# Kernel optimization log

Hardware: AMD Instinct MI355X
Metric: run time of the kernel (lower is better)

The kernel has to match this reference:

```python
import jax, jax.numpy as jnp
import numpy as np

N_EMBD = 768
N_HEAD = 12
HEAD_DIM = N_EMBD // N_HEAD


def setup_inputs() -> dict:
    key = jax.random.key(0)
    ks = jax.random.split(key, 9)
    s = 0.02
    return {
        "x": jax.random.normal(ks[0], (2, 4096, N_EMBD), dtype=jnp.float32),
        "Wq": jax.random.normal(ks[1], (N_EMBD, N_EMBD), dtype=jnp.float32) * s,
        "bq": jnp.zeros((N_EMBD,), dtype=jnp.float32),
        "Wk": jax.random.normal(ks[2], (N_EMBD, N_EMBD), dtype=jnp.float32) * s,
        "bk": jnp.zeros((N_EMBD,), dtype=jnp.float32),
        "Wv": jax.random.normal(ks[3], (N_EMBD, N_EMBD), dtype=jnp.float32) * s,
        "bv": jnp.zeros((N_EMBD,), dtype=jnp.float32),
        "Wo": jax.random.normal(ks[4], (N_EMBD, N_EMBD), dtype=jnp.float32) * s,
        "bo": jnp.zeros((N_EMBD,), dtype=jnp.float32),
    }


def reference(x, Wq, bq, Wk, bk, Wv, bv, Wo, bo):
    B, T, C = x.shape
    H, D = N_HEAD, HEAD_DIM
    # torch Linear: y = x @ W.T + b
    q = (x @ Wq.T + bq).reshape(B, T, H, D).transpose(0, 2, 1, 3)  # [B,H,T,D]
    k = (x @ Wk.T + bk).reshape(B, T, H, D).transpose(0, 2, 1, 3)
    v = (x @ Wv.T + bv).reshape(B, T, H, D).transpose(0, 2, 1, 3)
    scale = 1.0 / jnp.sqrt(jnp.float32(D))
    att = jnp.einsum("bhqd,bhkd->bhqk", q, k) * scale  # [B,H,T,T]
    causal = jnp.tril(jnp.ones((T, T), dtype=bool))
    att = jnp.where(causal[None, None], att, -jnp.inf)
    att = jax.nn.softmax(att, axis=-1)
    y = jnp.einsum("bhqk,bhkd->bhqd", att, v)
    y = y.transpose(0, 2, 1, 3).reshape(B, T, C)
    return y @ Wo.T + bo
```

## Files before the change

kernel.cpp:

```cpp
#include <hip/hip_runtime.h>

typedef __bf16 bf16_t;
typedef __bf16 bf16x4 __attribute__((ext_vector_type(4)));
typedef __bf16 bf16x8 __attribute__((ext_vector_type(8)));
typedef float  f32x4  __attribute__((ext_vector_type(4)));
typedef float  f32x16 __attribute__((ext_vector_type(16)));
typedef unsigned int u32;

#define MFMA16(a, b, c) __builtin_amdgcn_mfma_f32_16x16x32_bf16((a), (b), (c), 0, 0, 0)
#define MFMA32(a, b, c) __builtin_amdgcn_mfma_f32_32x32x16_bf16((a), (b), (c), 0, 0, 0)

__device__ __forceinline__ void gld_lds16(const bf16_t* g, bf16_t* l) {
  __builtin_amdgcn_global_load_lds((__attribute__((address_space(1))) void*)g,
                                   (__attribute__((address_space(3))) void*)l, 16, 0, 0);
}
__device__ __forceinline__ u32 cvt_pk_bf16(float lo, float hi) {
  u32 r;
  asm("v_cvt_pk_bf16_f32 %0, %1, %2" : "=v"(r) : "v"(lo), "v"(hi));
  return r;
}

__global__ void cast_f32_bf16(const float* __restrict__ s, bf16_t* __restrict__ d, int n) {
  int i = (blockIdx.x * blockDim.x + threadIdx.x) * 4;
  if (i >= n) return;
  float4 v = *(const float4*)(s + i);
  bf16x4 o;
  o[0] = (bf16_t)v.x; o[1] = (bf16_t)v.y; o[2] = (bf16_t)v.z; o[3] = (bf16_t)v.w;
  *(bf16x4*)(d + i) = o;
}

__global__ void prep_w(const float* __restrict__ Wq, const float* __restrict__ Wk,
                       const float* __restrict__ Wv, const float* __restrict__ Wo,
                       const float* __restrict__ bq, const float* __restrict__ bk,
                       const float* __restrict__ bv,
                       bf16_t* __restrict__ wqkv, bf16_t* __restrict__ wob,
                       float* __restrict__ qkvb) {
  const int NW = 768 * 768;
  const int t = blockIdx.x * 256 + threadIdx.x;
  const int i = t * 4;
  if (i < 3 * NW) {
    const float* s; int off;
    if (i < NW)          { s = Wq; off = i; }
    else if (i < 2 * NW) { s = Wk; off = i - NW; }
    else                 { s = Wv; off = i - 2 * NW; }
    float4 v = *(const float4*)(s + off);
    bf16x4 o;
    o[0] = (bf16_t)v.x; o[1] = (bf16_t)v.y; o[2] = (bf16_t)v.z; o[3] = (bf16_t)v.w;
    *(bf16x4*)(wqkv + i) = o;
  } else if (i < 4 * NW) {
    const int off = i - 3 * NW;
    float4 v = *(const float4*)(Wo + off);
    bf16x4 o;
    o[0] = (bf16_t)v.x; o[1] = (bf16_t)v.y; o[2] = (bf16_t)v.z; o[3] = (bf16_t)v.w;
    *(bf16x4*)(wob + off) = o;
  }
  if (t < 2304) qkvb[t] = t < 768 ? bq[t] : (t < 1536 ? bk[t - 768] : bv[t - 1536]);
}

__global__ __launch_bounds__(256) void gemm_qkv(
    const bf16_t* __restrict__ A, const bf16_t* __restrict__ B,
    const float* __restrict__ bias,
    bf16_t* __restrict__ qb, bf16_t* __restrict__ kb2, bf16_t* __restrict__ vtb) {
  __shared__ __align__(16) bf16_t As[128 * 64];
  __shared__ __align__(16) bf16_t Bs[128 * 64];
  const int K = 768;
  const int bm = blockIdx.x, bn = blockIdx.y;
  const int tid = threadIdx.x;
  const int w = tid >> 6, l = tid & 63, lg = l >> 4, ln = l & 15;
  const int wr = w >> 1, wc = w & 1;
  const int lr8 = l >> 3, lc8 = l & 7;
  const int region = (bn * 128) / 768;
  const int ln7 = ln & 7;
  f32x4 acc[4][4] = {};
  for (int kb = 0; kb < K / 64; ++kb) {
    const int k0 = kb * 64;
#pragma unroll
    for (int i = 0; i < 4; ++i) {
      const int row = w * 32 + i * 8 + lr8;
      const int so = k0 + ((lc8 ^ (row & 7)) << 3);
      gld_lds16(A + (size_t)(bm * 128 + row) * K + so, As + (w * 32 + i * 8) * 64 + l * 8);
      gld_lds16(B + (size_t)(bn * 128 + row) * K + so, Bs + (w * 32 + i * 8) * 64 + l * 8);
    }
    __syncthreads();
#pragma unroll
    for (int kk = 0; kk < 2; ++kk) {
      bf16x8 af[4], bfr[4];
#pragma unroll
      for (int m = 0; m < 4; ++m) {
        const int jc = ((kk * 4 + lg) ^ ln7) << 3;
        af[m]  = *(const bf16x8*)(As + (wr * 64 + m * 16 + ln) * 64 + jc);
        bfr[m] = *(const bf16x8*)(Bs + (wc * 64 + m * 16 + ln) * 64 + jc);
      }
      if (region != 2) {
#pragma unroll
        for (int m = 0; m < 4; ++m)
#pragma unroll
          for (int n = 0; n < 4; ++n) acc[m][n] = MFMA16(af[m], bfr[n], acc[m][n]);
      } else {
#pragma unroll
        for (int m = 0; m < 4; ++m)
#pragma unroll
          for (int n = 0; n < 4; ++n) acc[m][n] = MFMA16(bfr[n], af[m], acc[m][n]);
      }
    }
    __syncthreads();
  }
  if (region != 2) {
    const float scl = (region == 0) ? 0.18033688011112042f : 1.0f;
    bf16_t* dst = region == 0 ? qb : kb2;
#pragma unroll
    for (int m = 0; m < 4; ++m)
#pragma unroll
      for (int n = 0; n < 4; ++n)
#pragma unroll
        for (int j = 0; j < 4; ++j) {
          const int gm = bm * 128 + wr * 64 + m * 16 + lg * 4 + j;
          const int gn = bn * 128 + wc * 64 + n * 16 + ln;
          const float v = (acc[m][n][j] + bias[gn]) * scl;
          const int c = gn - region * 768;
          const int bb = gm >> 12, tt = gm & 4095;
          const int hh = c >> 6, d = c & 63;
          dst[((size_t)(bb * 12 + hh) * 4096 + tt) * 64 + d] = (bf16_t)v;
        }
  } else {
#pragma unroll
    for (int m = 0; m < 4; ++m)
#pragma unroll
      for (int n = 0; n < 4; ++n)
#pragma unroll
        for (int j = 0; j < 4; ++j) {
          const int gn = bn * 128 + wc * 64 + n * 16 + lg * 4 + j;
          const int gm = bm * 128 + wr * 64 + m * 16 + ln;
          const float v = acc[m][n][j] + bias[gn];
          const int c = gn - 1536;
          const int bb = gm >> 12, tt = gm & 4095;
          const int hh = c >> 6, d = c & 63;
          vtb[((size_t)(bb * 12 + hh) * 64 + d) * 4096 + tt] = (bf16_t)v;
        }
  }
}

__global__ __launch_bounds__(512) void attn_fwd(
    const bf16_t* __restrict__ q, const bf16_t* __restrict__ k,
    const bf16_t* __restrict__ vt, bf16_t* __restrict__ y) {
  __shared__ __align__(16) unsigned char SMEM[65536];
  bf16_t* Ks = (bf16_t*)SMEM;
  bf16_t* Vs = (bf16_t*)(SMEM + 32768);
  float*  osh = (float*)SMEM;
  float*  lsh = (float*)(SMEM + 32768);

  const int p = blockIdx.x;
  const int xcd = p & 7, slot = p >> 3;
  const int hb = xcd + 8 * (slot % 3);
  const int qt = 31 - slot / 3;
  const int tid = threadIdx.x;
  const int w = tid >> 6, l = tid & 63, lq = l & 31, lh = l >> 5;
  const int wq = w >> 1, wc = w & 1;
  const size_t hbo = (size_t)hb * (4096 * 64);
  const bf16_t* qh = q + hbo;
  const bf16_t* kh = k + hbo;
  const bf16_t* vh = vt + hbo;

  const int q0 = qt * 128 + wq * 32;
  const int qidx = q0 + lq;
  const int nst = qt + 1;

  const int sr = ((tid >> 8) << 5) | (tid & 31);
  const int sc = ((((tid >> 6) & 3) << 1) | ((tid >> 5) & 1)) << 3;
  const bf16_t* k0src = kh + ((size_t)sr * 64 + sc);
  const bf16_t* k1src = k0src + 4096;
  const bf16_t* v0src = vh + ((size_t)sr * 4096 + sc);
  const bf16_t* v1src = v0src + 64;

  bf16x8 qf[4];
#pragma unroll
  for (int ds = 0; ds < 4; ++ds)
    qf[ds] = *(const bf16x8*)(qh + (size_t)qidx * 64 + 16 * ds + 8 * lh);

  gld_lds16(k0src, Ks + tid * 8);
  gld_lds16(k1src, Ks + 4096 + tid * 8);
  gld_lds16(v0src, Vs + tid * 8);
  gld_lds16(v1src, Vs + 4096 + tid * 8);
  __syncthreads();

  f32x16 o0 = {}, o1 = {};
  float lsum = 0.f;

  int cur = 0;
  for (int i = 0; i < nst; ++i) {
    if (i + 1 < nst) {
      bf16_t* kd = Ks + (cur ^ 1) * 8192;
      bf16_t* vd = Vs + (cur ^ 1) * 8192;
      gld_lds16(k0src + 8192, kd + tid * 8);
      gld_lds16(k1src + 8192, kd + 4096 + tid * 8);
      gld_lds16(v0src + 128, vd + tid * 8);
      gld_lds16(v1src + 128, vd + 4096 + tid * 8);
    }
    k0src += 8192; k1src += 8192; v0src += 128; v1src += 128;
    const int t = 2 * i + wc;
    if (t * 64 <= q0 + 31) {
      const int kvb = t * 64;
      const bool diag = (kvb + 63 > q0);
      const bf16_t* KsW = Ks + (cur * 2 + wc) * 4096;
      const bf16_t* VsW = Vs + (cur * 2 + wc) * 4096;
      u32 pq[2][8];
#pragma unroll
      for (int kb = 0; kb < 2; ++kb) {
        f32x16 st = {};
        __builtin_amdgcn_s_setprio(1);
#pragma unroll
        for (int ds = 0; ds < 4; ++ds) {
          bf16x8 kf = *(const bf16x8*)(KsW + (kb * 4 + ds) * 512 + l * 8);
          st = MFMA32(kf, qf[ds], st);
        }
        __builtin_amdgcn_s_setprio(0);
        float pv[16];
#pragma unroll
        for (int r = 0; r < 16; ++r) pv[r] = __builtin_amdgcn_exp2f(st[r]);
        if (diag) {
          const int kb0 = kvb + kb * 32 + 4 * lh;
#pragma unroll
          for (int r = 0; r < 16; ++r)
            if (kb0 + (r & 3) + 8 * (r >> 2) > qidx) pv[r] = 0.f;
        }
#pragma unroll
        for (int r = 0; r < 16; ++r) lsum += pv[r];
#pragma unroll
        for (int g = 0; g < 8; ++g) pq[kb][g] = cvt_pk_bf16(pv[2 * g], pv[2 * g + 1]);
#pragma unroll
        for (int ks2 = 0; ks2 < 2; ++ks2) {
          asm("v_permlane32_swap_b32 %0, %1" : "+v"(pq[kb][4 * ks2 + 0]), "+v"(pq[kb][4 * ks2 + 2]));
          asm("v_permlane32_swap_b32 %0, %1" : "+v"(pq[kb][4 * ks2 + 1]), "+v"(pq[kb][4 * ks2 + 3]));
        }
      }
      __builtin_amdgcn_s_setprio(1);
#pragma unroll
      for (int ks = 0; ks < 4; ++ks) {
        bf16x8 pa = *(const bf16x8*)&pq[ks >> 1][(ks & 1) * 4];
        bf16x8 v0 = *(const bf16x8*)(VsW + ks * 512 + l * 8);
        bf16x8 v1 = *(const bf16x8*)(VsW + (4 + ks) * 512 + l * 8);
        o0 = MFMA32(pa, v0, o0);
        o1 = MFMA32(pa, v1, o1);
      }
      __builtin_amdgcn_s_setprio(0);
    }
    __syncthreads();
    cur ^= 1;
  }
  lsum += __shfl_xor(lsum, 32);

  if (wc == 1) {
#pragma unroll
    for (int r = 0; r < 16; ++r) {
      osh[wq * 2048 + r * 64 + l] = o0[r];
      osh[wq * 2048 + (16 + r) * 64 + l] = o1[r];
    }
    lsh[wq * 64 + l] = lsum;
  }
  __syncthreads();
  if (wc == 0) {
    lsum += lsh[wq * 64 + l];
#pragma unroll
    for (int r = 0; r < 16; ++r) {
      o0[r] += osh[wq * 2048 + r * 64 + l];
      o1[r] += osh[wq * 2048 + (16 + r) * 64 + l];
    }
    float linv[16];
#pragma unroll
    for (int r = 0; r < 16; ++r)
      linv[r] = 1.0f / __shfl(lsum, (r & 3) + 8 * (r >> 2) + 4 * lh);
    const int b = hb / 12, h = hb - b * 12;
#pragma unroll
    for (int r = 0; r < 16; ++r) {
      const int row = q0 + (r & 3) + 8 * (r >> 2) + 4 * lh;
      bf16_t* yr = y + ((size_t)b * 4096 + row) * 768 + h * 64 + lq;
      yr[0]  = (bf16_t)(o0[r] * linv[r]);
      yr[32] = (bf16_t)(o1[r] * linv[r]);
    }
  }
}

__global__ __launch_bounds__(256) void gemm_out(
    const bf16_t* __restrict__ A, const bf16_t* __restrict__ B,
    const float* __restrict__ bias, float* __restrict__ out) {
  __shared__ __align__(16) bf16_t As[128 * 64];
  __shared__ __align__(16) bf16_t Bs[128 * 64];
  const int K = 768;
  const int bm = blockIdx.x, bn = blockIdx.y;
  const int tid = threadIdx.x;
  const int w = tid >> 6, l = tid & 63, lg = l >> 4, ln = l & 15;
  const int wr = w >> 1, wc = w & 1;
  const int lr8 = l >> 3, lc8 = l & 7;
  const int ln7 = ln & 7;
  f32x4 acc[4][4] = {};
  for (int kb = 0; kb < K / 64; ++kb) {
    const int k0 = kb * 64;
#pragma unroll
    for (int i = 0; i < 4; ++i) {
      const int row = w * 32 + i * 8 + lr8;
      const int so = k0 + ((lc8 ^ (row & 7)) << 3);
      gld_lds16(A + (size_t)(bm * 128 + row) * K + so, As + (w * 32 + i * 8) * 64 + l * 8);
      gld_lds16(B + (size_t)(bn * 128 + row) * K + so, Bs + (w * 32 + i * 8) * 64 + l * 8);
    }
    __syncthreads();
#pragma unroll
    for (int kk = 0; kk < 2; ++kk) {
      bf16x8 af[4], bfr[4];
#pragma unroll
      for (int m = 0; m < 4; ++m) {
        const int jc = ((kk * 4 + lg) ^ ln7) << 3;
        af[m]  = *(const bf16x8*)(As + (wr * 64 + m * 16 + ln) * 64 + jc);
        bfr[m] = *(const bf16x8*)(Bs + (wc * 64 + m * 16 + ln) * 64 + jc);
      }
#pragma unroll
      for (int m = 0; m < 4; ++m)
#pragma unroll
        for (int n = 0; n < 4; ++n) acc[m][n] = MFMA16(af[m], bfr[n], acc[m][n]);
    }
    __syncthreads();
  }
  const int gn0 = bn * 128 + wc * 64;
#pragma unroll
  for (int m = 0; m < 4; ++m) {
#pragma unroll
    for (int n = 0; n < 4; ++n) {
#pragma unroll
      for (int j = 0; j < 4; ++j) {
        const int gm = bm * 128 + wr * 64 + m * 16 + lg * 4 + j;
        const int gn = gn0 + n * 16 + ln;
        out[(size_t)gm * 768 + gn] = acc[m][n][j] + bias[gn];
      }
    }
  }
}

extern "C" void kernel_launch(void* const* d_in, const int* in_sizes, int n_in,
                              void* d_out, int out_size, void* d_ws, size_t ws_size,
                              hipStream_t stream) {
  const float* x  = (const float*)d_in[0];
  const float* Wq = (const float*)d_in[1];
  const float* bq = (const float*)d_in[2];
  const float* Wk = (const float*)d_in[3];
  const float* bk = (const float*)d_in[4];
  const float* Wv = (const float*)d_in[5];
  const float* bv = (const float*)d_in[6];
  const float* Wo = (const float*)d_in[7];
  const float* bo = (const float*)d_in[8];
  float* out = (float*)d_out;

  const int M = 8192, C = 768, QKV = 2304;
  bf16_t* xb   = (bf16_t*)d_ws;
  bf16_t* wqkv = xb + (size_t)M * C;
  bf16_t* wob  = wqkv + (size_t)QKV * C;
  float*  qkvb = (float*)(wob + (size_t)C * C);
  bf16_t* qbuf = (bf16_t*)(qkvb + QKV);
  bf16_t* kbuf = qbuf + (size_t)M * C;
  bf16_t* vtb  = kbuf + (size_t)M * C;
  bf16_t* yb   = xb;

  cast_f32_bf16<<<6144, 256, 0, stream>>>(x, xb, M * C);
  prep_w<<<2304, 256, 0, stream>>>(Wq, Wk, Wv, Wo, bq, bk, bv, wqkv, wob, qkvb);

  gemm_qkv<<<dim3(64, 18), 256, 0, stream>>>(xb, wqkv, qkvb, qbuf, kbuf, vtb);
  attn_fwd<<<768, 512, 0, stream>>>(qbuf, kbuf, vtb, yb);
  gemm_out<<<dim3(64, 6), 256, 0, stream>>>(yb, wob, bo, out);
}
```

Before: 173.2 us.

## Drop split-KV wave pairs in attention; use 4 waves per block over all KV tiles

The attention kernel previously used 8 waves where pairs of waves split each 128-key stage between two 64-key halves, then reduced their partial outputs through shared memory. It now uses 4 waves per block, each covering a 32-row query slice, and walks every 64-key tile serially with a smaller double-buffered K/V staging area. This removes the cross-wave LDS reduction and final barrier and halves shared memory per block, which may allow more resident blocks. In exchange each wave does twice as many sequential iterations, with more barriers per block and less intra-block parallelism.

```diff
diff --git a/kernel.cpp b/kernel.cpp
--- a/kernel.cpp
+++ b/kernel.cpp
@@ -140,14 +140,11 @@
   }
 }
 
-__global__ __launch_bounds__(512) void attn_fwd(
+__global__ __launch_bounds__(256) void attn_fwd(
     const bf16_t* __restrict__ q, const bf16_t* __restrict__ k,
     const bf16_t* __restrict__ vt, bf16_t* __restrict__ y) {
-  __shared__ __align__(16) unsigned char SMEM[65536];
-  bf16_t* Ks = (bf16_t*)SMEM;
-  bf16_t* Vs = (bf16_t*)(SMEM + 32768);
-  float*  osh = (float*)SMEM;
-  float*  lsh = (float*)(SMEM + 32768);
+  __shared__ __align__(16) bf16_t Ks[2][4096];
+  __shared__ __align__(16) bf16_t Vs[2][4096];
 
   const int p = blockIdx.x;
   const int xcd = p & 7, slot = p >> 3;
@@ -155,54 +152,50 @@
   const int qt = 31 - slot / 3;
   const int tid = threadIdx.x;
   const int w = tid >> 6, l = tid & 63, lq = l & 31, lh = l >> 5;
-  const int wq = w >> 1, wc = w & 1;
   const size_t hbo = (size_t)hb * (4096 * 64);
   const bf16_t* qh = q + hbo;
   const bf16_t* kh = k + hbo;
   const bf16_t* vh = vt + hbo;
 
-  const int q0 = qt * 128 + wq * 32;
+  const int q0 = qt * 128 + w * 32;
   const int qidx = q0 + lq;
-  const int nst = qt + 1;
-
-  const int sr = ((tid >> 8) << 5) | (tid & 31);
-  const int sc = ((((tid >> 6) & 3) << 1) | ((tid >> 5) & 1)) << 3;
-  const bf16_t* k0src = kh + ((size_t)sr * 64 + sc);
-  const bf16_t* k1src = k0src + 4096;
-  const bf16_t* v0src = vh + ((size_t)sr * 4096 + sc);
-  const bf16_t* v1src = v0src + 64;
+  const int nst = 2 * qt + 2;
+
+  const int sr0 = tid & 31,           sc0 = ((((tid >> 6) & 3) << 1) | ((tid >> 5) & 1)) << 3;
+  const int sr1 = 32 | (tid & 31),    sc1 = sc0;
+  const bf16_t* ks0 = kh + ((size_t)sr0 * 64 + sc0);
+  const bf16_t* ks1 = kh + ((size_t)sr1 * 64 + sc1);
+  const bf16_t* vs0 = vh + ((size_t)sr0 * 4096 + sc0);
+  const bf16_t* vs1 = vh + ((size_t)sr1 * 4096 + sc1);
 
   bf16x8 qf[4];
 #pragma unroll
   for (int ds = 0; ds < 4; ++ds)
     qf[ds] = *(const bf16x8*)(qh + (size_t)qidx * 64 + 16 * ds + 8 * lh);
 
-  gld_lds16(k0src, Ks + tid * 8);
-  gld_lds16(k1src, Ks + 4096 + tid * 8);
-  gld_lds16(v0src, Vs + tid * 8);
-  gld_lds16(v1src, Vs + 4096 + tid * 8);
+  gld_lds16(ks0, &Ks[0][tid * 8]);
+  gld_lds16(ks1, &Ks[0][2048 + tid * 8]);
+  gld_lds16(vs0, &Vs[0][tid * 8]);
+  gld_lds16(vs1, &Vs[0][2048 + tid * 8]);
   __syncthreads();
 
   f32x16 o0 = {}, o1 = {};
   float lsum = 0.f;
 
   int cur = 0;
-  for (int i = 0; i < nst; ++i) {
-    if (i + 1 < nst) {
-      bf16_t* kd = Ks + (cur ^ 1) * 8192;
-      bf16_t* vd = Vs + (cur ^ 1) * 8192;
-      gld_lds16(k0src + 8192, kd + tid * 8);
-      gld_lds16(k1src + 8192, kd + 4096 + tid * 8);
-      gld_lds16(v0src + 128, vd + tid * 8);
-      gld_lds16(v1src + 128, vd + 4096 + tid * 8);
-    }
-    k0src += 8192; k1src += 8192; v0src += 128; v1src += 128;
-    const int t = 2 * i + wc;
-    if (t * 64 <= q0 + 31) {
-      const int kvb = t * 64;
+  for (int t = 0; t < nst; ++t) {
+    if (t + 1 < nst) {
+      gld_lds16(ks0 + 4096, &Ks[cur ^ 1][tid * 8]);
+      gld_lds16(ks1 + 4096, &Ks[cur ^ 1][2048 + tid * 8]);
+      gld_lds16(vs0 + 64, &Vs[cur ^ 1][tid * 8]);
+      gld_lds16(vs1 + 64, &Vs[cur ^ 1][2048 + tid * 8]);
+    }
+    ks0 += 4096; ks1 += 4096; vs0 += 64; vs1 += 64;
+    const int kvb = t * 64;
+    if (kvb <= q0 + 31) {
       const bool diag = (kvb + 63 > q0);
-      const bf16_t* KsW = Ks + (cur * 2 + wc) * 4096;
-      const bf16_t* VsW = Vs + (cur * 2 + wc) * 4096;
+      const bf16_t* KsW = &Ks[cur][0];
+      const bf16_t* VsW = &Vs[cur][0];
       u32 pq[2][8];
 #pragma unroll
       for (int kb = 0; kb < 2; ++kb) {
@@ -248,35 +241,17 @@
     cur ^= 1;
   }
   lsum += __shfl_xor(lsum, 32);
-
-  if (wc == 1) {
-#pragma unroll
-    for (int r = 0; r < 16; ++r) {
-      osh[wq * 2048 + r * 64 + l] = o0[r];
-      osh[wq * 2048 + (16 + r) * 64 + l] = o1[r];
-    }
-    lsh[wq * 64 + l] = lsum;
-  }
-  __syncthreads();
-  if (wc == 0) {
-    lsum += lsh[wq * 64 + l];
-#pragma unroll
-    for (int r = 0; r < 16; ++r) {
-      o0[r] += osh[wq * 2048 + r * 64 + l];
-      o1[r] += osh[wq * 2048 + (16 + r) * 64 + l];
-    }
-    float linv[16];
-#pragma unroll
-    for (int r = 0; r < 16; ++r)
-      linv[r] = 1.0f / __shfl(lsum, (r & 3) + 8 * (r >> 2) + 4 * lh);
-    const int b = hb / 12, h = hb - b * 12;
-#pragma unroll
-    for (int r = 0; r < 16; ++r) {
-      const int row = q0 + (r & 3) + 8 * (r >> 2) + 4 * lh;
-      bf16_t* yr = y + ((size_t)b * 4096 + row) * 768 + h * 64 + lq;
-      yr[0]  = (bf16_t)(o0[r] * linv[r]);
-      yr[32] = (bf16_t)(o1[r] * linv[r]);
-    }
+  float linv[16];
+#pragma unroll
+  for (int r = 0; r < 16; ++r)
+    linv[r] = 1.0f / __shfl(lsum, (r & 3) + 8 * (r >> 2) + 4 * lh);
+  const int b = hb / 12, h = hb - b * 12;
+#pragma unroll
+  for (int r = 0; r < 16; ++r) {
+    const int row = q0 + (r & 3) + 8 * (r >> 2) + 4 * lh;
+    bf16_t* yr = y + ((size_t)b * 4096 + row) * 768 + h * 64 + lq;
+    yr[0]  = (bf16_t)(o0[r] * linv[r]);
+    yr[32] = (bf16_t)(o1[r] * linv[r]);
   }
 }
 
@@ -362,6 +337,6 @@
   prep_w<<<2304, 256, 0, stream>>>(Wq, Wk, Wv, Wo, bq, bk, bv, wqkv, wob, qkvb);
 
   gemm_qkv<<<dim3(64, 18), 256, 0, stream>>>(xb, wqkv, qkvb, qbuf, kbuf, vtb);
-  attn_fwd<<<768, 512, 0, stream>>>(qbuf, kbuf, vtb, yb);
+  attn_fwd<<<768, 256, 0, stream>>>(qbuf, kbuf, vtb, yb);
   gemm_out<<<dim3(64, 6), 256, 0, stream>>>(yb, wob, bo, out);
 }
```

Result: slower. 207.1 us (+19.6%).

## Double-buffer LDS tiles in QKV and output projection GEMMs

Applied to the files above, without the earlier changes.

Both projection GEMMs now keep two 128x32 LDS buffers per operand and issue the global-to-LDS loads for the next K-slice before computing on the current one. Each iteration has a single barrier instead of two, and the load latency is meant to overlap with the MFMA work. The K-step drops from 64 to 32, so there are twice as many iterations with less compute in each. The XOR swizzle is changed to match the 32-wide rows. Whether the loads actually overlap depends on the compiler's vmcnt waits around the one barrier per iteration.

```diff
diff --git a/kernel.cpp b/kernel.cpp
--- a/kernel.cpp
+++ b/kernel.cpp
@@ -61,47 +61,54 @@
     const bf16_t* __restrict__ A, const bf16_t* __restrict__ B,
     const float* __restrict__ bias,
     bf16_t* __restrict__ qb, bf16_t* __restrict__ kb2, bf16_t* __restrict__ vtb) {
-  __shared__ __align__(16) bf16_t As[128 * 64];
-  __shared__ __align__(16) bf16_t Bs[128 * 64];
-  const int K = 768;
+  __shared__ __align__(16) bf16_t As[2][128 * 32];
+  __shared__ __align__(16) bf16_t Bs[2][128 * 32];
+  const int K = 768, NKB = 24;
   const int bm = blockIdx.x, bn = blockIdx.y;
   const int tid = threadIdx.x;
   const int w = tid >> 6, l = tid & 63, lg = l >> 4, ln = l & 15;
   const int wr = w >> 1, wc = w & 1;
-  const int lr8 = l >> 3, lc8 = l & 7;
   const int region = (bn * 128) / 768;
-  const int ln7 = ln & 7;
+  const int srow = tid >> 2, sch = tid & 3;
+  const int scol = (sch ^ ((srow >> 1) & 3)) << 3;
+  const bf16_t* aSrc0 = A + (size_t)(bm * 128 + srow) * K + scol;
+  const bf16_t* aSrc1 = A + (size_t)(bm * 128 + 64 + srow) * K + scol;
+  const bf16_t* bSrc0 = B + (size_t)(bn * 128 + srow) * K + scol;
+  const bf16_t* bSrc1 = B + (size_t)(bn * 128 + 64 + srow) * K + scol;
   f32x4 acc[4][4] = {};
-  for (int kb = 0; kb < K / 64; ++kb) {
-    const int k0 = kb * 64;
-#pragma unroll
-    for (int i = 0; i < 4; ++i) {
-      const int row = w * 32 + i * 8 + lr8;
-      const int so = k0 + ((lc8 ^ (row & 7)) << 3);
-      gld_lds16(A + (size_t)(bm * 128 + row) * K + so, As + (w * 32 + i * 8) * 64 + l * 8);
-      gld_lds16(B + (size_t)(bn * 128 + row) * K + so, Bs + (w * 32 + i * 8) * 64 + l * 8);
-    }
-    __syncthreads();
-#pragma unroll
-    for (int kk = 0; kk < 2; ++kk) {
-      bf16x8 af[4], bfr[4];
-#pragma unroll
-      for (int m = 0; m < 4; ++m) {
-        const int jc = ((kk * 4 + lg) ^ ln7) << 3;
-        af[m]  = *(const bf16x8*)(As + (wr * 64 + m * 16 + ln) * 64 + jc);
-        bfr[m] = *(const bf16x8*)(Bs + (wc * 64 + m * 16 + ln) * 64 + jc);
-      }
-      if (region != 2) {
-#pragma unroll
-        for (int m = 0; m < 4; ++m)
-#pragma unroll
-          for (int n = 0; n < 4; ++n) acc[m][n] = MFMA16(af[m], bfr[n], acc[m][n]);
-      } else {
-#pragma unroll
-        for (int m = 0; m < 4; ++m)
-#pragma unroll
-          for (int n = 0; n < 4; ++n) acc[m][n] = MFMA16(bfr[n], af[m], acc[m][n]);
-      }
+  gld_lds16(aSrc0, &As[0][tid * 8]);
+  gld_lds16(aSrc1, &As[0][(256 + tid) * 8]);
+  gld_lds16(bSrc0, &Bs[0][tid * 8]);
+  gld_lds16(bSrc1, &Bs[0][(256 + tid) * 8]);
+  aSrc0 += 32; aSrc1 += 32; bSrc0 += 32; bSrc1 += 32;
+  __syncthreads();
+  for (int kb = 0; kb < NKB; ++kb) {
+    const int cur = kb & 1;
+    if (kb + 1 < NKB) {
+      gld_lds16(aSrc0, &As[cur ^ 1][tid * 8]);
+      gld_lds16(aSrc1, &As[cur ^ 1][(256 + tid) * 8]);
+      gld_lds16(bSrc0, &Bs[cur ^ 1][tid * 8]);
+      gld_lds16(bSrc1, &Bs[cur ^ 1][(256 + tid) * 8]);
+      aSrc0 += 32; aSrc1 += 32; bSrc0 += 32; bSrc1 += 32;
+    }
+    bf16x8 af[4], bfr[4];
+#pragma unroll
+    for (int m = 0; m < 4; ++m) {
+      const int ra = wr * 64 + m * 16 + ln;
+      const int rb = wc * 64 + m * 16 + ln;
+      af[m]  = *(const bf16x8*)(&As[cur][ra * 32 + ((lg ^ ((ra >> 1) & 3)) << 3)]);
+      bfr[m] = *(const bf16x8*)(&Bs[cur][rb * 32 + ((lg ^ ((rb >> 1) & 3)) << 3)]);
+    }
+    if (region != 2) {
+#pragma unroll
+      for (int m = 0; m < 4; ++m)
+#pragma unroll
+        for (int n = 0; n < 4; ++n) acc[m][n] = MFMA16(af[m], bfr[n], acc[m][n]);
+    } else {
+#pragma unroll
+      for (int m = 0; m < 4; ++m)
+#pragma unroll
+        for (int n = 0; n < 4; ++n) acc[m][n] = MFMA16(bfr[n], af[m], acc[m][n]);
     }
     __syncthreads();
   }
@@ -283,40 +290,47 @@
 __global__ __launch_bounds__(256) void gemm_out(
     const bf16_t* __restrict__ A, const bf16_t* __restrict__ B,
     const float* __restrict__ bias, float* __restrict__ out) {
-  __shared__ __align__(16) bf16_t As[128 * 64];
-  __shared__ __align__(16) bf16_t Bs[128 * 64];
-  const int K = 768;
+  __shared__ __align__(16) bf16_t As[2][128 * 32];
+  __shared__ __align__(16) bf16_t Bs[2][128 * 32];
+  const int K = 768, NKB = 24;
   const int bm = blockIdx.x, bn = blockIdx.y;
   const int tid = threadIdx.x;
   const int w = tid >> 6, l = tid & 63, lg = l >> 4, ln = l & 15;
   const int wr = w >> 1, wc = w & 1;
-  const int lr8 = l >> 3, lc8 = l & 7;
-  const int ln7 = ln & 7;
+  const int srow = tid >> 2, sch = tid & 3;
+  const int scol = (sch ^ ((srow >> 1) & 3)) << 3;
+  const bf16_t* aSrc0 = A + (size_t)(bm * 128 + srow) * K + scol;
+  const bf16_t* aSrc1 = A + (size_t)(bm * 128 + 64 + srow) * K + scol;
+  const bf16_t* bSrc0 = B + (size_t)(bn * 128 + srow) * K + scol;
+  const bf16_t* bSrc1 = B + (size_t)(bn * 128 + 64 + srow) * K + scol;
   f32x4 acc[4][4] = {};
-  for (int kb = 0; kb < K / 64; ++kb) {
-    const int k0 = kb * 64;
-#pragma unroll
-    for (int i = 0; i < 4; ++i) {
-      const int row = w * 32 + i * 8 + lr8;
-      const int so = k0 + ((lc8 ^ (row & 7)) << 3);
-      gld_lds16(A + (size_t)(bm * 128 + row) * K + so, As + (w * 32 + i * 8) * 64 + l * 8);
-      gld_lds16(B + (size_t)(bn * 128 + row) * K + so, Bs + (w * 32 + i * 8) * 64 + l * 8);
-    }
-    __syncthreads();
-#pragma unroll
-    for (int kk = 0; kk < 2; ++kk) {
-      bf16x8 af[4], bfr[4];
-#pragma unroll
-      for (int m = 0; m < 4; ++m) {
-        const int jc = ((kk * 4 + lg) ^ ln7) << 3;
-        af[m]  = *(const bf16x8*)(As + (wr * 64 + m * 16 + ln) * 64 + jc);
-        bfr[m] = *(const bf16x8*)(Bs + (wc * 64 + m * 16 + ln) * 64 + jc);
-      }
-#pragma unroll
-      for (int m = 0; m < 4; ++m)
-#pragma unroll
-        for (int n = 0; n < 4; ++n) acc[m][n] = MFMA16(af[m], bfr[n], acc[m][n]);
-    }
+  gld_lds16(aSrc0, &As[0][tid * 8]);
+  gld_lds16(aSrc1, &As[0][(256 + tid) * 8]);
+  gld_lds16(bSrc0, &Bs[0][tid * 8]);
+  gld_lds16(bSrc1, &Bs[0][(256 + tid) * 8]);
+  aSrc0 += 32; aSrc1 += 32; bSrc0 += 32; bSrc1 += 32;
+  __syncthreads();
+  for (int kb = 0; kb < NKB; ++kb) {
+    const int cur = kb & 1;
+    if (kb + 1 < NKB) {
+      gld_lds16(aSrc0, &As[cur ^ 1][tid * 8]);
+      gld_lds16(aSrc1, &As[cur ^ 1][(256 + tid) * 8]);
+      gld_lds16(bSrc0, &Bs[cur ^ 1][tid * 8]);
+      gld_lds16(bSrc1, &Bs[cur ^ 1][(256 + tid) * 8]);
+      aSrc0 += 32; aSrc1 += 32; bSrc0 += 32; bSrc1 += 32;
+    }
+    bf16x8 af[4], bfr[4];
+#pragma unroll
+    for (int m = 0; m < 4; ++m) {
+      const int ra = wr * 64 + m * 16 + ln;
+      const int rb = wc * 64 + m * 16 + ln;
+      af[m]  = *(const bf16x8*)(&As[cur][ra * 32 + ((lg ^ ((ra >> 1) & 3)) << 3)]);
+      bfr[m] = *(const bf16x8*)(&Bs[cur][rb * 32 + ((lg ^ ((rb >> 1) & 3)) << 3)]);
+    }
+#pragma unroll
+    for (int m = 0; m < 4; ++m)
+#pragma unroll
+      for (int n = 0; n < 4; ++n) acc[m][n] = MFMA16(af[m], bfr[n], acc[m][n]);
     __syncthreads();
   }
   const int gn0 = bn * 128 + wc * 64;
```

Result: slower. 181.5 us (+4.8%).
